# Kernel optimization log

Measured on AMD Instinct MI355X. Metric: run time of the kernel, lower is better.

Reference implementation:

```python
import jax, jax.numpy as jnp
import numpy as np

USER_VOCAB = 1_000_000
MOVIE_VOCAB = 100_000
EMB_DIM = 64
BATCH = 65536
H1, H2 = 256, 128  # over_arch_layer_sizes


def setup_inputs() -> dict:
    key = jax.random.key(0)
    ks = jax.random.split(key, 10)
    inv = 1.0 / np.sqrt(EMB_DIM)
    return {
        "user_ids": jax.random.randint(ks[0], (BATCH,), 0, USER_VOCAB),
        "movie_ids": jax.random.randint(ks[1], (BATCH,), 0, MOVIE_VOCAB),
        "emb_user": jax.random.normal(ks[2], (USER_VOCAB, EMB_DIM), jnp.float32) * inv,
        "emb_movie": jax.random.normal(ks[3], (MOVIE_VOCAB, EMB_DIM), jnp.float32) * inv,
        "W1": jax.random.normal(ks[4], (EMB_DIM, H1), jnp.float32) * (1.0 / np.sqrt(EMB_DIM)),
        "b1": jnp.zeros((H1,), jnp.float32),
        "W2": jax.random.normal(ks[5], (H1, H2), jnp.float32) * (1.0 / np.sqrt(H1)),
        "b2": jnp.zeros((H2,), jnp.float32),
        "W3": jax.random.normal(ks[6], (H2, 1), jnp.float32) * (1.0 / np.sqrt(H2)),
        "b3": jnp.zeros((1,), jnp.float32),
    }


def reference(user_ids, movie_ids, emb_user, emb_movie, W1, b1, W2, b2, W3, b3):
    B = user_ids.shape[0]
    # sparse gather per feature (hotness = 1)
    eu = emb_user[user_ids]    # [B, D]
    em = emb_movie[movie_ids]  # [B, D]
    # concat jagged outputs along rows, matching torch.cat(..., dim=0)
    x = jnp.concatenate([eu, em], axis=0)  # [2B, D]
    h = jax.nn.relu(x @ W1 + b1)
    h = jax.nn.relu(h @ W2 + b2)
    p = h @ W3 + b3                        # [2B, 1]
    # view(num_features, batch).t().sum(-1) -> sum over features per sample
    return p.reshape(2, B).sum(axis=0)     # [B]
```

## Files before the change

### kernel.cpp

```cpp
#include <hip/hip_runtime.h>


typedef __attribute__((ext_vector_type(8))) short bf16x8;
typedef __attribute__((ext_vector_type(16))) float f32x16;
typedef __attribute__((ext_vector_type(4))) float f32x4n;

__device__ __forceinline__ unsigned int cvt_pk(float lo, float hi) {
  unsigned int r;
  asm("v_cvt_pk_bf16_f32 %0, %1, %2" : "=v"(r) : "v"(lo), "v"(hi));
  return r;
}

__global__ __launch_bounds__(512, 2) void movielens_mlp(
    const int* __restrict__ uids, const int* __restrict__ mids,
    const float* __restrict__ EU, const float* __restrict__ EM,
    const float* __restrict__ W1, const float* __restrict__ B1,
    const float* __restrict__ W2, const float* __restrict__ B2,
    const float* __restrict__ W3, const float* __restrict__ B3,
    float* __restrict__ out) {
  __shared__ __align__(16) unsigned short w1f[32 * 512];
  __shared__ __align__(16) unsigned short w2f[64 * 512];

  const int tid = threadIdx.x;
  const int lane = tid & 63, wv = tid >> 6;
  const int m32 = lane & 31, H = lane >> 5;
  const int sbase = blockIdx.x * 256 + wv * 32;
  const int sid = sbase + m32;

  const int uid = uids[sid];
  const int mid = mids[sid];

  const int cq = tid & 7, bb = (tid >> 3) & 1, hh = (tid >> 4) & 1;

  float4 w1r[2][4];
#pragma unroll
  for (int i = 0; i < 2; ++i) {
    const int fi = (tid >> 5) + 16 * i;
    const int ct = fi >> 2, kk = fi & 3;
    const float* s = W1 + (16 * kk + 8 * hh + 4 * bb) * 256 + 32 * ct + 4 * cq;
    w1r[i][0] = *(const float4*)(s);
    w1r[i][1] = *(const float4*)(s + 256);
    w1r[i][2] = *(const float4*)(s + 512);
    w1r[i][3] = *(const float4*)(s + 768);
  }
  float4 w2r[2][4];
  auto w2_load = [&](int pass, float4 r[4]) {
    const int f2 = (tid >> 5) + 16 * pass;
    const int ks = f2 >> 2, n2 = f2 & 3;
    const float* s = W2 + (16 * ks + 8 * hh + 4 * bb) * 128 + 32 * n2 + 4 * cq;
    r[0] = *(const float4*)(s);
    r[1] = *(const float4*)(s + 128);
    r[2] = *(const float4*)(s + 256);
    r[3] = *(const float4*)(s + 384);
  };
  w2_load(0, w2r[0]);
  w2_load(1, w2r[1]);

  const float* rowU = EU + (size_t)uid * 64;
  const float* rowM = EM + (size_t)mid * 64;
  f32x4n xr[2][4][2];
#pragma unroll
  for (int kk = 0; kk < 4; ++kk) {
    xr[0][kk][0] = __builtin_nontemporal_load((const f32x4n*)(rowU + 16 * kk + 8 * H));
    xr[0][kk][1] = __builtin_nontemporal_load((const f32x4n*)(rowU + 16 * kk + 8 * H + 4));
    xr[1][kk][0] = __builtin_nontemporal_load((const f32x4n*)(rowM + 16 * kk + 8 * H));
    xr[1][kk][1] = __builtin_nontemporal_load((const f32x4n*)(rowM + 16 * kk + 8 * H + 4));
  }

  const int w1slot0 = 32 * hh + 16 * (cq >> 2) + 8 * (cq & 1) + 4 * ((cq >> 1) & 1);
#pragma unroll
  for (int i = 0; i < 2; ++i) {
    const int fi = (tid >> 5) + 16 * i;
    const float c0[4] = {w1r[i][0].x, w1r[i][0].y, w1r[i][0].z, w1r[i][0].w};
    const float c1[4] = {w1r[i][1].x, w1r[i][1].y, w1r[i][1].z, w1r[i][1].w};
    const float c2[4] = {w1r[i][2].x, w1r[i][2].y, w1r[i][2].z, w1r[i][2].w};
    const float c3[4] = {w1r[i][3].x, w1r[i][3].y, w1r[i][3].z, w1r[i][3].w};
#pragma unroll
    for (int s = 0; s < 4; ++s) {
      uint2 pk;
      pk.x = cvt_pk(c0[s], c1[s]);
      pk.y = cvt_pk(c2[s], c3[s]);
      *(uint2*)&w1f[fi * 512 + (w1slot0 + s) * 8 + 4 * bb] = pk;
    }
  }
  auto w2_write = [&](int pass, const float4 r[4]) {
    const int f2 = (tid >> 5) + 16 * pass;
    const int slot0 = 32 * hh + 4 * cq;
    const float c0[4] = {r[0].x, r[0].y, r[0].z, r[0].w};
    const float c1[4] = {r[1].x, r[1].y, r[1].z, r[1].w};
    const float c2[4] = {r[2].x, r[2].y, r[2].z, r[2].w};
    const float c3[4] = {r[3].x, r[3].y, r[3].z, r[3].w};
#pragma unroll
    for (int s = 0; s < 4; ++s) {
      uint2 pk;
      pk.x = cvt_pk(c0[s], c1[s]);
      pk.y = cvt_pk(c2[s], c3[s]);
      *(uint2*)&w2f[f2 * 512 + (slot0 + s) * 8 + 4 * bb] = pk;
    }
  };
  w2_write(0, w2r[0]);
  __syncthreads();

  bf16x8 xf[2][4];
#pragma unroll
  for (int t = 0; t < 2; ++t)
#pragma unroll
    for (int kk = 0; kk < 4; ++kk) {
      const f32x4n a = xr[t][kk][0], b = xr[t][kk][1];
      uint4 w;
      w.x = cvt_pk(a.x, a.y);
      w.y = cvt_pk(a.z, a.w);
      w.z = cvt_pk(b.x, b.y);
      w.w = cvt_pk(b.z, b.w);
      xf[t][kk] = __builtin_bit_cast(bf16x8, w);
    }

  f32x16 acc2[2][4];
#pragma unroll
  for (int n2 = 0; n2 < 4; ++n2)
#pragma unroll
    for (int rq = 0; rq < 4; ++rq) {
      const float4 bq = *(const float4*)(B2 + 32 * n2 + 8 * rq + 4 * H);
      const float bv[4] = {bq.x, bq.y, bq.z, bq.w};
#pragma unroll
      for (int s = 0; s < 4; ++s) {
        acc2[0][n2][4 * rq + s] = bv[s];
        acc2[1][n2][4 * rq + s] = bv[s];
      }
    }

  bf16x8 a1[4];
#pragma unroll
  for (int kk = 0; kk < 4; ++kk)
    a1[kk] = *(const bf16x8*)&w1f[kk * 512 + lane * 8];

#pragma unroll
  for (int ct = 0; ct < 8; ++ct) {
    const float4 q0 = *(const float4*)(B1 + 32 * ct + 8 * H);
    const float4 q1 = *(const float4*)(B1 + 32 * ct + 8 * H + 4);
    const float4 q2 = *(const float4*)(B1 + 32 * ct + 8 * H + 16);
    const float4 q3 = *(const float4*)(B1 + 32 * ct + 8 * H + 20);
    f32x16 binit;
    binit[0] = q0.x; binit[1] = q0.y; binit[2] = q0.z; binit[3] = q0.w;
    binit[4] = q1.x; binit[5] = q1.y; binit[6] = q1.z; binit[7] = q1.w;
    binit[8] = q2.x; binit[9] = q2.y; binit[10] = q2.z; binit[11] = q2.w;
    binit[12] = q3.x; binit[13] = q3.y; binit[14] = q3.z; binit[15] = q3.w;

    f32x16 acc1a = binit;
#pragma unroll
    for (int kk = 0; kk < 4; ++kk)
      acc1a = __builtin_amdgcn_mfma_f32_32x32x16_bf16(a1[kk], xf[0][kk], acc1a, 0, 0, 0);
    uint4 lo0, hi0;
    lo0.x = cvt_pk(fmaxf(acc1a[0], 0.f), fmaxf(acc1a[1], 0.f));
    lo0.y = cvt_pk(fmaxf(acc1a[2], 0.f), fmaxf(acc1a[3], 0.f));
    lo0.z = cvt_pk(fmaxf(acc1a[4], 0.f), fmaxf(acc1a[5], 0.f));
    lo0.w = cvt_pk(fmaxf(acc1a[6], 0.f), fmaxf(acc1a[7], 0.f));
    hi0.x = cvt_pk(fmaxf(acc1a[8], 0.f), fmaxf(acc1a[9], 0.f));
    hi0.y = cvt_pk(fmaxf(acc1a[10], 0.f), fmaxf(acc1a[11], 0.f));
    hi0.z = cvt_pk(fmaxf(acc1a[12], 0.f), fmaxf(acc1a[13], 0.f));
    hi0.w = cvt_pk(fmaxf(acc1a[14], 0.f), fmaxf(acc1a[15], 0.f));

    f32x16 acc1b = binit;
#pragma unroll
    for (int kk = 0; kk < 4; ++kk)
      acc1b = __builtin_amdgcn_mfma_f32_32x32x16_bf16(a1[kk], xf[1][kk], acc1b, 0, 0, 0);
    uint4 lo1, hi1;
    lo1.x = cvt_pk(fmaxf(acc1b[0], 0.f), fmaxf(acc1b[1], 0.f));
    lo1.y = cvt_pk(fmaxf(acc1b[2], 0.f), fmaxf(acc1b[3], 0.f));
    lo1.z = cvt_pk(fmaxf(acc1b[4], 0.f), fmaxf(acc1b[5], 0.f));
    lo1.w = cvt_pk(fmaxf(acc1b[6], 0.f), fmaxf(acc1b[7], 0.f));
    hi1.x = cvt_pk(fmaxf(acc1b[8], 0.f), fmaxf(acc1b[9], 0.f));
    hi1.y = cvt_pk(fmaxf(acc1b[10], 0.f), fmaxf(acc1b[11], 0.f));
    hi1.z = cvt_pk(fmaxf(acc1b[12], 0.f), fmaxf(acc1b[13], 0.f));
    hi1.w = cvt_pk(fmaxf(acc1b[14], 0.f), fmaxf(acc1b[15], 0.f));

    if (ct < 7) {
#pragma unroll
      for (int kk = 0; kk < 4; ++kk)
        a1[kk] = *(const bf16x8*)&w1f[((ct + 1) * 4 + kk) * 512 + lane * 8];
    }

#pragma unroll
    for (int q = 0; q < 4; ++q) {
      const bf16x8 wlo = *(const bf16x8*)&w2f[(8 * ct + q) * 512 + lane * 8];
      acc2[0][q] = __builtin_amdgcn_mfma_f32_32x32x16_bf16(
          wlo, __builtin_bit_cast(bf16x8, lo0), acc2[0][q], 0, 0, 0);
      acc2[1][q] = __builtin_amdgcn_mfma_f32_32x32x16_bf16(
          wlo, __builtin_bit_cast(bf16x8, lo1), acc2[1][q], 0, 0, 0);
    }
#pragma unroll
    for (int q = 0; q < 4; ++q) {
      const bf16x8 whi = *(const bf16x8*)&w2f[(8 * ct + 4 + q) * 512 + lane * 8];
      acc2[0][q] = __builtin_amdgcn_mfma_f32_32x32x16_bf16(
          whi, __builtin_bit_cast(bf16x8, hi0), acc2[0][q], 0, 0, 0);
      acc2[1][q] = __builtin_amdgcn_mfma_f32_32x32x16_bf16(
          whi, __builtin_bit_cast(bf16x8, hi1), acc2[1][q], 0, 0, 0);
    }

    if (ct == 0) {
      w2_write(1, w2r[1]);
      w2_load(2, w2r[0]);
      __syncthreads();
    } else if (ct == 2) {
      w2_write(2, w2r[0]);
      w2_load(3, w2r[1]);
      __syncthreads();
    } else if (ct == 4) {
      w2_write(3, w2r[1]);
      __syncthreads();
    }
  }

  float part = 0.f;
#pragma unroll
  for (int n2 = 0; n2 < 4; ++n2) {
#pragma unroll
    for (int rq = 0; rq < 4; ++rq) {
      const float4 wq = *(const float4*)(W3 + 32 * n2 + 8 * rq + 4 * H);
      const float wv4[4] = {wq.x, wq.y, wq.z, wq.w};
#pragma unroll
      for (int s = 0; s < 4; ++s) {
        part += fmaxf(acc2[0][n2][4 * rq + s], 0.f) * wv4[s];
        part += fmaxf(acc2[1][n2][4 * rq + s], 0.f) * wv4[s];
      }
    }
  }
  part += __shfl_xor(part, 32, 64);
  if (lane < 32) {
    __builtin_nontemporal_store(part + 2.f * B3[0], out + sbase + lane);
  }
}

extern "C" void kernel_launch(void* const* d_in, const int* in_sizes, int n_in,
                              void* d_out, int out_size, void* d_ws, size_t ws_size,
                              hipStream_t stream) {
  const int* uids = (const int*)d_in[0];
  const int* mids = (const int*)d_in[1];
  const float* EU = (const float*)d_in[2];
  const float* EM = (const float*)d_in[3];
  const float* W1 = (const float*)d_in[4];
  const float* B1 = (const float*)d_in[5];
  const float* W2 = (const float*)d_in[6];
  const float* B2 = (const float*)d_in[7];
  const float* W3 = (const float*)d_in[8];
  const float* B3 = (const float*)d_in[9];
  float* out = (float*)d_out;

  const int B = in_sizes[0];
  const int nblk = B / 256;
  hipLaunchKernelGGL(movielens_mlp, dim3(nblk), dim3(512), 0, stream,
                     uids, mids, EU, EM, W1, B1, W2, B2, W3, B3, out);
}
```

Before: 26.49 us.

## Load all weights upfront and process user and movie passes sequentially

All W1/W2 fragments are now loaded and staged into shared memory before a single barrier, replacing the staged W2 writes and extra barriers interleaved with the first layer loop. The two embedding streams are no longer computed together. A run_pass lambda processes user rows fully, then movie rows, which halves live accumulator registers, and the movie gather is deferred so it can overlap the user pass. Nontemporal loads and stores are replaced by ordinary ones. The trade is less MFMA interleaving between independent chains and a longer serial dependency per wave, in exchange for lower register pressure and fewer barriers.

Result: slower. 28.69 us (+8.3%).

```diff
diff --git a/kernel.cpp b/kernel.cpp
--- a/kernel.cpp
+++ b/kernel.cpp
@@ -3,7 +3,6 @@
 
 typedef __attribute__((ext_vector_type(8))) short bf16x8;
 typedef __attribute__((ext_vector_type(16))) float f32x16;
-typedef __attribute__((ext_vector_type(4))) float f32x4n;
 
 __device__ __forceinline__ unsigned int cvt_pk(float lo, float hi) {
   unsigned int r;
@@ -32,49 +31,44 @@
 
   const int cq = tid & 7, bb = (tid >> 3) & 1, hh = (tid >> 4) & 1;
 
-  float4 w1r[2][4];
+  float4 wr[6][4];
 #pragma unroll
   for (int i = 0; i < 2; ++i) {
     const int fi = (tid >> 5) + 16 * i;
     const int ct = fi >> 2, kk = fi & 3;
     const float* s = W1 + (16 * kk + 8 * hh + 4 * bb) * 256 + 32 * ct + 4 * cq;
-    w1r[i][0] = *(const float4*)(s);
-    w1r[i][1] = *(const float4*)(s + 256);
-    w1r[i][2] = *(const float4*)(s + 512);
-    w1r[i][3] = *(const float4*)(s + 768);
-  }
-  float4 w2r[2][4];
-  auto w2_load = [&](int pass, float4 r[4]) {
-    const int f2 = (tid >> 5) + 16 * pass;
+    wr[i][0] = *(const float4*)(s);
+    wr[i][1] = *(const float4*)(s + 256);
+    wr[i][2] = *(const float4*)(s + 512);
+    wr[i][3] = *(const float4*)(s + 768);
+  }
+#pragma unroll
+  for (int i = 2; i < 6; ++i) {
+    const int f2 = (tid >> 5) + 16 * (i - 2);
     const int ks = f2 >> 2, n2 = f2 & 3;
     const float* s = W2 + (16 * ks + 8 * hh + 4 * bb) * 128 + 32 * n2 + 4 * cq;
-    r[0] = *(const float4*)(s);
-    r[1] = *(const float4*)(s + 128);
-    r[2] = *(const float4*)(s + 256);
-    r[3] = *(const float4*)(s + 384);
-  };
-  w2_load(0, w2r[0]);
-  w2_load(1, w2r[1]);
+    wr[i][0] = *(const float4*)(s);
+    wr[i][1] = *(const float4*)(s + 128);
+    wr[i][2] = *(const float4*)(s + 256);
+    wr[i][3] = *(const float4*)(s + 384);
+  }
 
   const float* rowU = EU + (size_t)uid * 64;
-  const float* rowM = EM + (size_t)mid * 64;
-  f32x4n xr[2][4][2];
-#pragma unroll
-  for (int kk = 0; kk < 4; ++kk) {
-    xr[0][kk][0] = __builtin_nontemporal_load((const f32x4n*)(rowU + 16 * kk + 8 * H));
-    xr[0][kk][1] = __builtin_nontemporal_load((const f32x4n*)(rowU + 16 * kk + 8 * H + 4));
-    xr[1][kk][0] = __builtin_nontemporal_load((const f32x4n*)(rowM + 16 * kk + 8 * H));
-    xr[1][kk][1] = __builtin_nontemporal_load((const f32x4n*)(rowM + 16 * kk + 8 * H + 4));
+  float4 xu[4][2];
+#pragma unroll
+  for (int kk = 0; kk < 4; ++kk) {
+    xu[kk][0] = *(const float4*)(rowU + 16 * kk + 8 * H);
+    xu[kk][1] = *(const float4*)(rowU + 16 * kk + 8 * H + 4);
   }
 
   const int w1slot0 = 32 * hh + 16 * (cq >> 2) + 8 * (cq & 1) + 4 * ((cq >> 1) & 1);
 #pragma unroll
   for (int i = 0; i < 2; ++i) {
     const int fi = (tid >> 5) + 16 * i;
-    const float c0[4] = {w1r[i][0].x, w1r[i][0].y, w1r[i][0].z, w1r[i][0].w};
-    const float c1[4] = {w1r[i][1].x, w1r[i][1].y, w1r[i][1].z, w1r[i][1].w};
-    const float c2[4] = {w1r[i][2].x, w1r[i][2].y, w1r[i][2].z, w1r[i][2].w};
-    const float c3[4] = {w1r[i][3].x, w1r[i][3].y, w1r[i][3].z, w1r[i][3].w};
+    const float c0[4] = {wr[i][0].x, wr[i][0].y, wr[i][0].z, wr[i][0].w};
+    const float c1[4] = {wr[i][1].x, wr[i][1].y, wr[i][1].z, wr[i][1].w};
+    const float c2[4] = {wr[i][2].x, wr[i][2].y, wr[i][2].z, wr[i][2].w};
+    const float c3[4] = {wr[i][3].x, wr[i][3].y, wr[i][3].z, wr[i][3].w};
 #pragma unroll
     for (int s = 0; s < 4; ++s) {
       uint2 pk;
@@ -83,13 +77,14 @@
       *(uint2*)&w1f[fi * 512 + (w1slot0 + s) * 8 + 4 * bb] = pk;
     }
   }
-  auto w2_write = [&](int pass, const float4 r[4]) {
-    const int f2 = (tid >> 5) + 16 * pass;
+#pragma unroll
+  for (int i = 2; i < 6; ++i) {
+    const int f2 = (tid >> 5) + 16 * (i - 2);
     const int slot0 = 32 * hh + 4 * cq;
-    const float c0[4] = {r[0].x, r[0].y, r[0].z, r[0].w};
-    const float c1[4] = {r[1].x, r[1].y, r[1].z, r[1].w};
-    const float c2[4] = {r[2].x, r[2].y, r[2].z, r[2].w};
-    const float c3[4] = {r[3].x, r[3].y, r[3].z, r[3].w};
+    const float c0[4] = {wr[i][0].x, wr[i][0].y, wr[i][0].z, wr[i][0].w};
+    const float c1[4] = {wr[i][1].x, wr[i][1].y, wr[i][1].z, wr[i][1].w};
+    const float c2[4] = {wr[i][2].x, wr[i][2].y, wr[i][2].z, wr[i][2].w};
+    const float c3[4] = {wr[i][3].x, wr[i][3].y, wr[i][3].z, wr[i][3].w};
 #pragma unroll
     for (int s = 0; s < 4; ++s) {
       uint2 pk;
@@ -97,138 +92,123 @@
       pk.y = cvt_pk(c2[s], c3[s]);
       *(uint2*)&w2f[f2 * 512 + (slot0 + s) * 8 + 4 * bb] = pk;
     }
+  }
+
+  const float* rowM = EM + (size_t)mid * 64;
+  float4 xm[4][2];
+#pragma unroll
+  for (int kk = 0; kk < 4; ++kk) {
+    xm[kk][0] = *(const float4*)(rowM + 16 * kk + 8 * H);
+    xm[kk][1] = *(const float4*)(rowM + 16 * kk + 8 * H + 4);
+  }
+
+  bf16x8 xfu[4];
+#pragma unroll
+  for (int kk = 0; kk < 4; ++kk) {
+    const float4 a = xu[kk][0], b = xu[kk][1];
+    uint4 w;
+    w.x = cvt_pk(a.x, a.y);
+    w.y = cvt_pk(a.z, a.w);
+    w.z = cvt_pk(b.x, b.y);
+    w.w = cvt_pk(b.z, b.w);
+    xfu[kk] = __builtin_bit_cast(bf16x8, w);
+  }
+  __syncthreads();
+
+  auto run_pass = [&](const bf16x8 xf[4]) -> float {
+    f32x16 acc2[4];
+#pragma unroll
+    for (int n2 = 0; n2 < 4; ++n2)
+#pragma unroll
+      for (int rq = 0; rq < 4; ++rq) {
+        const float4 bq = *(const float4*)(B2 + 32 * n2 + 8 * rq + 4 * H);
+        acc2[n2][4 * rq + 0] = bq.x;
+        acc2[n2][4 * rq + 1] = bq.y;
+        acc2[n2][4 * rq + 2] = bq.z;
+        acc2[n2][4 * rq + 3] = bq.w;
+      }
+    bf16x8 a1[4];
+#pragma unroll
+    for (int kk = 0; kk < 4; ++kk)
+      a1[kk] = *(const bf16x8*)&w1f[kk * 512 + lane * 8];
+
+#pragma unroll
+    for (int ct = 0; ct < 8; ++ct) {
+      const float4 q0 = *(const float4*)(B1 + 32 * ct + 8 * H);
+      const float4 q1 = *(const float4*)(B1 + 32 * ct + 8 * H + 4);
+      const float4 q2 = *(const float4*)(B1 + 32 * ct + 8 * H + 16);
+      const float4 q3 = *(const float4*)(B1 + 32 * ct + 8 * H + 20);
+      f32x16 acc1;
+      acc1[0] = q0.x;  acc1[1] = q0.y;  acc1[2] = q0.z;  acc1[3] = q0.w;
+      acc1[4] = q1.x;  acc1[5] = q1.y;  acc1[6] = q1.z;  acc1[7] = q1.w;
+      acc1[8] = q2.x;  acc1[9] = q2.y;  acc1[10] = q2.z; acc1[11] = q2.w;
+      acc1[12] = q3.x; acc1[13] = q3.y; acc1[14] = q3.z; acc1[15] = q3.w;
+#pragma unroll
+      for (int kk = 0; kk < 4; ++kk)
+        acc1 = __builtin_amdgcn_mfma_f32_32x32x16_bf16(a1[kk], xf[kk], acc1, 0, 0, 0);
+
+      uint4 lo, hi;
+      lo.x = cvt_pk(fmaxf(acc1[0], 0.f), fmaxf(acc1[1], 0.f));
+      lo.y = cvt_pk(fmaxf(acc1[2], 0.f), fmaxf(acc1[3], 0.f));
+      lo.z = cvt_pk(fmaxf(acc1[4], 0.f), fmaxf(acc1[5], 0.f));
+      lo.w = cvt_pk(fmaxf(acc1[6], 0.f), fmaxf(acc1[7], 0.f));
+      hi.x = cvt_pk(fmaxf(acc1[8], 0.f), fmaxf(acc1[9], 0.f));
+      hi.y = cvt_pk(fmaxf(acc1[10], 0.f), fmaxf(acc1[11], 0.f));
+      hi.z = cvt_pk(fmaxf(acc1[12], 0.f), fmaxf(acc1[13], 0.f));
+      hi.w = cvt_pk(fmaxf(acc1[14], 0.f), fmaxf(acc1[15], 0.f));
+
+      if (ct < 7) {
+#pragma unroll
+        for (int kk = 0; kk < 4; ++kk)
+          a1[kk] = *(const bf16x8*)&w1f[((ct + 1) * 4 + kk) * 512 + lane * 8];
+      }
+
+#pragma unroll
+      for (int q = 0; q < 4; ++q) {
+        const bf16x8 wlo = *(const bf16x8*)&w2f[(8 * ct + q) * 512 + lane * 8];
+        acc2[q] = __builtin_amdgcn_mfma_f32_32x32x16_bf16(
+            wlo, __builtin_bit_cast(bf16x8, lo), acc2[q], 0, 0, 0);
+      }
+#pragma unroll
+      for (int q = 0; q < 4; ++q) {
+        const bf16x8 whi = *(const bf16x8*)&w2f[(8 * ct + 4 + q) * 512 + lane * 8];
+        acc2[q] = __builtin_amdgcn_mfma_f32_32x32x16_bf16(
+            whi, __builtin_bit_cast(bf16x8, hi), acc2[q], 0, 0, 0);
+      }
+    }
+
+    float part = 0.f;
+#pragma unroll
+    for (int n2 = 0; n2 < 4; ++n2)
+#pragma unroll
+      for (int rq = 0; rq < 4; ++rq) {
+        const float4 wq = *(const float4*)(W3 + 32 * n2 + 8 * rq + 4 * H);
+        part += fmaxf(acc2[n2][4 * rq + 0], 0.f) * wq.x +
+                fmaxf(acc2[n2][4 * rq + 1], 0.f) * wq.y +
+                fmaxf(acc2[n2][4 * rq + 2], 0.f) * wq.z +
+                fmaxf(acc2[n2][4 * rq + 3], 0.f) * wq.w;
+      }
+    return part;
   };
-  w2_write(0, w2r[0]);
-  __syncthreads();
-
-  bf16x8 xf[2][4];
-#pragma unroll
-  for (int t = 0; t < 2; ++t)
-#pragma unroll
-    for (int kk = 0; kk < 4; ++kk) {
-      const f32x4n a = xr[t][kk][0], b = xr[t][kk][1];
-      uint4 w;
-      w.x = cvt_pk(a.x, a.y);
-      w.y = cvt_pk(a.z, a.w);
-      w.z = cvt_pk(b.x, b.y);
-      w.w = cvt_pk(b.z, b.w);
-      xf[t][kk] = __builtin_bit_cast(bf16x8, w);
-    }
-
-  f32x16 acc2[2][4];
-#pragma unroll
-  for (int n2 = 0; n2 < 4; ++n2)
-#pragma unroll
-    for (int rq = 0; rq < 4; ++rq) {
-      const float4 bq = *(const float4*)(B2 + 32 * n2 + 8 * rq + 4 * H);
-      const float bv[4] = {bq.x, bq.y, bq.z, bq.w};
-#pragma unroll
-      for (int s = 0; s < 4; ++s) {
-        acc2[0][n2][4 * rq + s] = bv[s];
-        acc2[1][n2][4 * rq + s] = bv[s];
-      }
-    }
-
-  bf16x8 a1[4];
-#pragma unroll
-  for (int kk = 0; kk < 4; ++kk)
-    a1[kk] = *(const bf16x8*)&w1f[kk * 512 + lane * 8];
-
-#pragma unroll
-  for (int ct = 0; ct < 8; ++ct) {
-    const float4 q0 = *(const float4*)(B1 + 32 * ct + 8 * H);
-    const float4 q1 = *(const float4*)(B1 + 32 * ct + 8 * H + 4);
-    const float4 q2 = *(const float4*)(B1 + 32 * ct + 8 * H + 16);
-    const float4 q3 = *(const float4*)(B1 + 32 * ct + 8 * H + 20);
-    f32x16 binit;
-    binit[0] = q0.x; binit[1] = q0.y; binit[2] = q0.z; binit[3] = q0.w;
-    binit[4] = q1.x; binit[5] = q1.y; binit[6] = q1.z; binit[7] = q1.w;
-    binit[8] = q2.x; binit[9] = q2.y; binit[10] = q2.z; binit[11] = q2.w;
-    binit[12] = q3.x; binit[13] = q3.y; binit[14] = q3.z; binit[15] = q3.w;
-
-    f32x16 acc1a = binit;
-#pragma unroll
-    for (int kk = 0; kk < 4; ++kk)
-      acc1a = __builtin_amdgcn_mfma_f32_32x32x16_bf16(a1[kk], xf[0][kk], acc1a, 0, 0, 0);
-    uint4 lo0, hi0;
-    lo0.x = cvt_pk(fmaxf(acc1a[0], 0.f), fmaxf(acc1a[1], 0.f));
-    lo0.y = cvt_pk(fmaxf(acc1a[2], 0.f), fmaxf(acc1a[3], 0.f));
-    lo0.z = cvt_pk(fmaxf(acc1a[4], 0.f), fmaxf(acc1a[5], 0.f));
-    lo0.w = cvt_pk(fmaxf(acc1a[6], 0.f), fmaxf(acc1a[7], 0.f));
-    hi0.x = cvt_pk(fmaxf(acc1a[8], 0.f), fmaxf(acc1a[9], 0.f));
-    hi0.y = cvt_pk(fmaxf(acc1a[10], 0.f), fmaxf(acc1a[11], 0.f));
-    hi0.z = cvt_pk(fmaxf(acc1a[12], 0.f), fmaxf(acc1a[13], 0.f));
-    hi0.w = cvt_pk(fmaxf(acc1a[14], 0.f), fmaxf(acc1a[15], 0.f));
-
-    f32x16 acc1b = binit;
-#pragma unroll
-    for (int kk = 0; kk < 4; ++kk)
-      acc1b = __builtin_amdgcn_mfma_f32_32x32x16_bf16(a1[kk], xf[1][kk], acc1b, 0, 0, 0);
-    uint4 lo1, hi1;
-    lo1.x = cvt_pk(fmaxf(acc1b[0], 0.f), fmaxf(acc1b[1], 0.f));
-    lo1.y = cvt_pk(fmaxf(acc1b[2], 0.f), fmaxf(acc1b[3], 0.f));
-    lo1.z = cvt_pk(fmaxf(acc1b[4], 0.f), fmaxf(acc1b[5], 0.f));
-    lo1.w = cvt_pk(fmaxf(acc1b[6], 0.f), fmaxf(acc1b[7], 0.f));
-    hi1.x = cvt_pk(fmaxf(acc1b[8], 0.f), fmaxf(acc1b[9], 0.f));
-    hi1.y = cvt_pk(fmaxf(acc1b[10], 0.f), fmaxf(acc1b[11], 0.f));
-    hi1.z = cvt_pk(fmaxf(acc1b[12], 0.f), fmaxf(acc1b[13], 0.f));
-    hi1.w = cvt_pk(fmaxf(acc1b[14], 0.f), fmaxf(acc1b[15], 0.f));
-
-    if (ct < 7) {
-#pragma unroll
-      for (int kk = 0; kk < 4; ++kk)
-        a1[kk] = *(const bf16x8*)&w1f[((ct + 1) * 4 + kk) * 512 + lane * 8];
-    }
-
-#pragma unroll
-    for (int q = 0; q < 4; ++q) {
-      const bf16x8 wlo = *(const bf16x8*)&w2f[(8 * ct + q) * 512 + lane * 8];
-      acc2[0][q] = __builtin_amdgcn_mfma_f32_32x32x16_bf16(
-          wlo, __builtin_bit_cast(bf16x8, lo0), acc2[0][q], 0, 0, 0);
-      acc2[1][q] = __builtin_amdgcn_mfma_f32_32x32x16_bf16(
-          wlo, __builtin_bit_cast(bf16x8, lo1), acc2[1][q], 0, 0, 0);
-    }
-#pragma unroll
-    for (int q = 0; q < 4; ++q) {
-      const bf16x8 whi = *(const bf16x8*)&w2f[(8 * ct + 4 + q) * 512 + lane * 8];
-      acc2[0][q] = __builtin_amdgcn_mfma_f32_32x32x16_bf16(
-          whi, __builtin_bit_cast(bf16x8, hi0), acc2[0][q], 0, 0, 0);
-      acc2[1][q] = __builtin_amdgcn_mfma_f32_32x32x16_bf16(
-          whi, __builtin_bit_cast(bf16x8, hi1), acc2[1][q], 0, 0, 0);
-    }
-
-    if (ct == 0) {
-      w2_write(1, w2r[1]);
-      w2_load(2, w2r[0]);
-      __syncthreads();
-    } else if (ct == 2) {
-      w2_write(2, w2r[0]);
-      w2_load(3, w2r[1]);
-      __syncthreads();
-    } else if (ct == 4) {
-      w2_write(3, w2r[1]);
-      __syncthreads();
-    }
-  }
-
-  float part = 0.f;
-#pragma unroll
-  for (int n2 = 0; n2 < 4; ++n2) {
-#pragma unroll
-    for (int rq = 0; rq < 4; ++rq) {
-      const float4 wq = *(const float4*)(W3 + 32 * n2 + 8 * rq + 4 * H);
-      const float wv4[4] = {wq.x, wq.y, wq.z, wq.w};
-#pragma unroll
-      for (int s = 0; s < 4; ++s) {
-        part += fmaxf(acc2[0][n2][4 * rq + s], 0.f) * wv4[s];
-        part += fmaxf(acc2[1][n2][4 * rq + s], 0.f) * wv4[s];
-      }
-    }
-  }
+
+  const float part_u = run_pass(xfu);
+
+  bf16x8 xfm[4];
+#pragma unroll
+  for (int kk = 0; kk < 4; ++kk) {
+    const float4 a = xm[kk][0], b = xm[kk][1];
+    uint4 w;
+    w.x = cvt_pk(a.x, a.y);
+    w.y = cvt_pk(a.z, a.w);
+    w.z = cvt_pk(b.x, b.y);
+    w.w = cvt_pk(b.z, b.w);
+    xfm[kk] = __builtin_bit_cast(bf16x8, w);
+  }
+  const float part_m = run_pass(xfm);
+
+  float part = part_u + part_m;
   part += __shfl_xor(part, 32, 64);
-  if (lane < 32) {
-    __builtin_nontemporal_store(part + 2.f * B3[0], out + sbase + lane);
-  }
+  if (lane < 32) out[sbase + lane] = part + 2.f * B3[0];
 }
 
 extern "C" void kernel_launch(void* const* d_in, const int* in_sizes, int n_in,
```

## Load all W2 weights upfront and drop staged writes and mid-loop barriers

Applied to the files above, without the earlier changes.

Loads all W1 and W2 fp32 weight tiles into registers at kernel start, converts them to bf16 and writes the whole of W2 to shared memory before a single barrier. This removes the staged W2 writes and the three __syncthreads interleaved with the layer-1/layer-2 MFMA loop. The barrier becomes a raw s_waitcnt lgkmcnt(0)+s_barrier with a sched_barrier, the ct loop is only partially unrolled (2), and the embedding loads and output store become ordinary instead of nontemporal. In exchange, register pressure rises from holding 24 float4 weights at once. Less overlap of weight loading with compute could lengthen the prologue.

After: 21.79 us (median of 2 runs). -17.7%, faster.

```diff
diff --git a/kernel.cpp b/kernel.cpp
--- a/kernel.cpp
+++ b/kernel.cpp
@@ -3,7 +3,6 @@
 
 typedef __attribute__((ext_vector_type(8))) short bf16x8;
 typedef __attribute__((ext_vector_type(16))) float f32x16;
-typedef __attribute__((ext_vector_type(4))) float f32x4n;
 
 __device__ __forceinline__ unsigned int cvt_pk(float lo, float hi) {
   unsigned int r;
@@ -32,49 +31,47 @@
 
   const int cq = tid & 7, bb = (tid >> 3) & 1, hh = (tid >> 4) & 1;
 
-  float4 w1r[2][4];
+  float4 wr[6][4];
 #pragma unroll
   for (int i = 0; i < 2; ++i) {
     const int fi = (tid >> 5) + 16 * i;
     const int ct = fi >> 2, kk = fi & 3;
     const float* s = W1 + (16 * kk + 8 * hh + 4 * bb) * 256 + 32 * ct + 4 * cq;
-    w1r[i][0] = *(const float4*)(s);
-    w1r[i][1] = *(const float4*)(s + 256);
-    w1r[i][2] = *(const float4*)(s + 512);
-    w1r[i][3] = *(const float4*)(s + 768);
-  }
-  float4 w2r[2][4];
-  auto w2_load = [&](int pass, float4 r[4]) {
-    const int f2 = (tid >> 5) + 16 * pass;
+    wr[i][0] = *(const float4*)(s);
+    wr[i][1] = *(const float4*)(s + 256);
+    wr[i][2] = *(const float4*)(s + 512);
+    wr[i][3] = *(const float4*)(s + 768);
+  }
+#pragma unroll
+  for (int i = 2; i < 6; ++i) {
+    const int f2 = (tid >> 5) + 16 * (i - 2);
     const int ks = f2 >> 2, n2 = f2 & 3;
     const float* s = W2 + (16 * ks + 8 * hh + 4 * bb) * 128 + 32 * n2 + 4 * cq;
-    r[0] = *(const float4*)(s);
-    r[1] = *(const float4*)(s + 128);
-    r[2] = *(const float4*)(s + 256);
-    r[3] = *(const float4*)(s + 384);
-  };
-  w2_load(0, w2r[0]);
-  w2_load(1, w2r[1]);
+    wr[i][0] = *(const float4*)(s);
+    wr[i][1] = *(const float4*)(s + 128);
+    wr[i][2] = *(const float4*)(s + 256);
+    wr[i][3] = *(const float4*)(s + 384);
+  }
 
   const float* rowU = EU + (size_t)uid * 64;
   const float* rowM = EM + (size_t)mid * 64;
-  f32x4n xr[2][4][2];
+  float4 xr[2][4][2];
 #pragma unroll
   for (int kk = 0; kk < 4; ++kk) {
-    xr[0][kk][0] = __builtin_nontemporal_load((const f32x4n*)(rowU + 16 * kk + 8 * H));
-    xr[0][kk][1] = __builtin_nontemporal_load((const f32x4n*)(rowU + 16 * kk + 8 * H + 4));
-    xr[1][kk][0] = __builtin_nontemporal_load((const f32x4n*)(rowM + 16 * kk + 8 * H));
-    xr[1][kk][1] = __builtin_nontemporal_load((const f32x4n*)(rowM + 16 * kk + 8 * H + 4));
+    xr[0][kk][0] = *(const float4*)(rowU + 16 * kk + 8 * H);
+    xr[0][kk][1] = *(const float4*)(rowU + 16 * kk + 8 * H + 4);
+    xr[1][kk][0] = *(const float4*)(rowM + 16 * kk + 8 * H);
+    xr[1][kk][1] = *(const float4*)(rowM + 16 * kk + 8 * H + 4);
   }
 
   const int w1slot0 = 32 * hh + 16 * (cq >> 2) + 8 * (cq & 1) + 4 * ((cq >> 1) & 1);
 #pragma unroll
   for (int i = 0; i < 2; ++i) {
     const int fi = (tid >> 5) + 16 * i;
-    const float c0[4] = {w1r[i][0].x, w1r[i][0].y, w1r[i][0].z, w1r[i][0].w};
-    const float c1[4] = {w1r[i][1].x, w1r[i][1].y, w1r[i][1].z, w1r[i][1].w};
-    const float c2[4] = {w1r[i][2].x, w1r[i][2].y, w1r[i][2].z, w1r[i][2].w};
-    const float c3[4] = {w1r[i][3].x, w1r[i][3].y, w1r[i][3].z, w1r[i][3].w};
+    const float c0[4] = {wr[i][0].x, wr[i][0].y, wr[i][0].z, wr[i][0].w};
+    const float c1[4] = {wr[i][1].x, wr[i][1].y, wr[i][1].z, wr[i][1].w};
+    const float c2[4] = {wr[i][2].x, wr[i][2].y, wr[i][2].z, wr[i][2].w};
+    const float c3[4] = {wr[i][3].x, wr[i][3].y, wr[i][3].z, wr[i][3].w};
 #pragma unroll
     for (int s = 0; s < 4; ++s) {
       uint2 pk;
@@ -83,13 +80,14 @@
       *(uint2*)&w1f[fi * 512 + (w1slot0 + s) * 8 + 4 * bb] = pk;
     }
   }
-  auto w2_write = [&](int pass, const float4 r[4]) {
-    const int f2 = (tid >> 5) + 16 * pass;
+#pragma unroll
+  for (int i = 2; i < 6; ++i) {
+    const int f2 = (tid >> 5) + 16 * (i - 2);
     const int slot0 = 32 * hh + 4 * cq;
-    const float c0[4] = {r[0].x, r[0].y, r[0].z, r[0].w};
-    const float c1[4] = {r[1].x, r[1].y, r[1].z, r[1].w};
-    const float c2[4] = {r[2].x, r[2].y, r[2].z, r[2].w};
-    const float c3[4] = {r[3].x, r[3].y, r[3].z, r[3].w};
+    const float c0[4] = {wr[i][0].x, wr[i][0].y, wr[i][0].z, wr[i][0].w};
+    const float c1[4] = {wr[i][1].x, wr[i][1].y, wr[i][1].z, wr[i][1].w};
+    const float c2[4] = {wr[i][2].x, wr[i][2].y, wr[i][2].z, wr[i][2].w};
+    const float c3[4] = {wr[i][3].x, wr[i][3].y, wr[i][3].z, wr[i][3].w};
 #pragma unroll
     for (int s = 0; s < 4; ++s) {
       uint2 pk;
@@ -97,16 +95,17 @@
       pk.y = cvt_pk(c2[s], c3[s]);
       *(uint2*)&w2f[f2 * 512 + (slot0 + s) * 8 + 4 * bb] = pk;
     }
-  };
-  w2_write(0, w2r[0]);
-  __syncthreads();
+  }
+
+  asm volatile("s_waitcnt lgkmcnt(0)\n\ts_barrier" ::: "memory");
+  __builtin_amdgcn_sched_barrier(0);
 
   bf16x8 xf[2][4];
 #pragma unroll
   for (int t = 0; t < 2; ++t)
 #pragma unroll
     for (int kk = 0; kk < 4; ++kk) {
-      const f32x4n a = xr[t][kk][0], b = xr[t][kk][1];
+      const float4 a = xr[t][kk][0], b = xr[t][kk][1];
       uint4 w;
       w.x = cvt_pk(a.x, a.y);
       w.y = cvt_pk(a.z, a.w);
@@ -134,7 +133,7 @@
   for (int kk = 0; kk < 4; ++kk)
     a1[kk] = *(const bf16x8*)&w1f[kk * 512 + lane * 8];
 
-#pragma unroll
+#pragma unroll 2
   for (int ct = 0; ct < 8; ++ct) {
     const float4 q0 = *(const float4*)(B1 + 32 * ct + 8 * H);
     const float4 q1 = *(const float4*)(B1 + 32 * ct + 8 * H + 4);
@@ -196,19 +195,6 @@
       acc2[1][q] = __builtin_amdgcn_mfma_f32_32x32x16_bf16(
           whi, __builtin_bit_cast(bf16x8, hi1), acc2[1][q], 0, 0, 0);
     }
-
-    if (ct == 0) {
-      w2_write(1, w2r[1]);
-      w2_load(2, w2r[0]);
-      __syncthreads();
-    } else if (ct == 2) {
-      w2_write(2, w2r[0]);
-      w2_load(3, w2r[1]);
-      __syncthreads();
-    } else if (ct == 4) {
-      w2_write(3, w2r[1]);
-      __syncthreads();
-    }
   }
 
   float part = 0.f;
@@ -226,9 +212,7 @@
     }
   }
   part += __shfl_xor(part, 32, 64);
-  if (lane < 32) {
-    __builtin_nontemporal_store(part + 2.f * B3[0], out + sbase + lane);
-  }
+  if (lane < 32) out[sbase + lane] = part + 2.f * B3[0];
 }
 
 extern "C" void kernel_launch(void* const* d_in, const int* in_sizes, int n_in,
```
